# Performance work log

Measured on AMD Instinct MI355X. Metric: run time of the kernel, lower is better.

## Reference

```python
import jax, jax.numpy as jnp
import numpy as np

N = 20000      # nodes
E = 640000     # edges
R = 90         # relations
IN_F = 128     # raw feature dim
HID = 64       # hidden_channels
OUT = 32       # out_channels of conv2
NCLASS = 4
NB = 35        # num_bases (conv1)
EPS = 1e-16    # PyG softmax epsilon


def setup_inputs() -> dict:
    key = jax.random.key(0)
    ks = jax.random.split(key, 16)
    s = 0.1
    return {
        "x": jax.random.normal(ks[0], (N, IN_F), jnp.float32),
        "edge_index": jax.random.randint(ks[1], (2, E), 0, N, jnp.int32),
        "edge_type": jax.random.randint(ks[2], (E,), 0, R, jnp.int32),
        "edge_attr": jax.random.normal(ks[3], (E, 16), jnp.float32),
        # lin1: in_channels -> hidden (no bias)
        "lin1_w": jax.random.normal(ks[4], (IN_F, HID), jnp.float32) * s,
        # conv1: basis decomposition, heads=2, out=20, dim=2 -> H*O=40, H*dim=4
        "att1": jax.random.normal(ks[5], (R, NB), jnp.float32) * s,
        "basis1": jax.random.normal(ks[6], (NB, HID, 40), jnp.float32) * s,
        "q1": jax.random.normal(ks[7], (40, 4), jnp.float32) * s,
        "k1": jax.random.normal(ks[8], (40, 4), jnp.float32) * s,
        "wmod1": jnp.ones((20,), jnp.float32),            # mod='additive' weight (init ones)
        "bias1": jnp.zeros((80,), jnp.float32),            # concat bias: H*dim*O = 80
        # conv2: block-diagonal, in=80, blocks=2, H*O=64, H*dim=2
        "w2": jax.random.normal(ks[9], (R, 2, 40, 32), jnp.float32) * s,
        "q2": jax.random.normal(ks[10], (64, 2), jnp.float32) * s,
        "k2": jax.random.normal(ks[11], (64, 2), jnp.float32) * s,
        "lin_edge_w": jax.random.normal(ks[12], (16, 64), jnp.float32) * s,
        "e2": jax.random.normal(ks[13], (64, 2), jnp.float32) * s,
        # lin2: 2*out -> nclass
        "lin2_w": jax.random.normal(ks[14], (2 * OUT, NCLASS), jnp.float32) * s,
        "lin2_b": jnp.zeros((NCLASS,), jnp.float32),
    }


def segment_softmax(alpha, seg, num_segments):
    # PyG softmax: exp(x - detach(segment_max)) / (segment_sum + 1e-16)
    m = jax.ops.segment_max(alpha, seg, num_segments=num_segments)
    e = jnp.exp(alpha - jax.lax.stop_gradient(m)[seg])
    ssum = jax.ops.segment_sum(e, seg, num_segments=num_segments)
    return e / (ssum[seg] + EPS)


def rgat_forward(x, edge_index, edge_type, edge_attr, lin1_w, att1, basis1,
                 q1, k1, wmod1, bias1, w2, q2, k2, lin_edge_w, e2, lin2_w, lin2_b):
    src, dst = edge_index[0], edge_index[1]   # x_j = x[src], x_i = x[dst]
    n = x.shape[0]
    e = src.shape[0]

    h = x @ lin1_w                            # [N, HID]

    # ---- conv1: basis decomposition, within-relation, multiplicative attn, mod='additive'
    w = jnp.einsum('rb,bio->rio', att1, basis1)          # [R, HID, 40]
    xw = jnp.einsum('ni,rio->rno', h, w)                 # [R, N, 40] (all-relation transform)
    outj = xw[edge_type, src]                            # [E, 40]
    outi = xw[edge_type, dst]                            # [E, 40]
    qi = outi @ q1                                       # [E, 4]
    kj = outj @ k1                                       # [E, 4]
    alpha = qi * kj                                      # multiplicative-self-attention
    seg = dst.astype(jnp.int32) * R + edge_type          # within-relation softmax groups
    alpha = segment_softmax(alpha, seg, n * R)           # [E, 4]
    outj4 = outj.reshape(e, 2, 1, 20)                    # [E, H, 1, O]
    hmod = wmod1 * jnp.broadcast_to(outj4, (e, 2, 2, 20))  # mod='additive' term
    msg = outj4 * alpha.reshape(e, 2, 2, 1) + hmod       # [E, H, dim, O]
    agg = jax.ops.segment_sum(msg, dst, num_segments=n)  # [N, 2, 2, 20]
    h1 = agg.reshape(n, 80) + bias1
    h1 = jax.nn.relu(h1)

    # ---- conv2: block-diagonal, across-relation, additive attn, edge features, no bias
    xb = h1.reshape(n, 2, 40)
    xw2 = jnp.einsum('nbc,rbcd->rnbd', xb, w2).reshape(R, n, 64)  # [R, N, 64]
    outj = xw2[edge_type, src]                           # [E, 64]
    outi = xw2[edge_type, dst]
    qi = outi @ q2                                       # [E, 2]
    kj = outj @ k2
    ae = (edge_attr @ lin_edge_w) @ e2                   # [E, 2]
    alpha = jax.nn.leaky_relu(qi + kj + ae, 0.2)         # additive-self-attention
    alpha = segment_softmax(alpha, dst, n)               # across-relation
    msg = alpha.reshape(e, 2, 1) * outj.reshape(e, 2, 32)
    h2 = jax.ops.segment_sum(msg, dst, num_segments=n).reshape(n, 64)

    out = h2 @ lin2_w + lin2_b
    return jax.nn.log_softmax(out, axis=-1)


def reference(x, edge_index, edge_type, edge_attr, lin1_w, att1, basis1, q1, k1,
              wmod1, bias1, w2, q2, k2, lin_edge_w, e2, lin2_w, lin2_b):
    return rgat_forward(x, edge_index, edge_type, edge_attr, lin1_w, att1, basis1,
                        q1, k1, wmod1, bias1, w2, q2, k2, lin_edge_w, e2, lin2_w, lin2_b)
```

## Files before the change

### kernel.cpp

```cpp
#include <hip/hip_runtime.h>
#include <math.h>

constexpr int NN   = 20000;
constexpr int EE   = 640000;
constexpr int RR   = 90;
constexpr int INF_ = 128;
constexpr int HID  = 64;
constexpr float EPS = 1e-16f;
constexpr int E2   = 646144;

typedef unsigned short u16;
typedef _Float16 f16;
typedef __attribute__((ext_vector_type(8))) _Float16 f16x8;
typedef __attribute__((ext_vector_type(4))) _Float16 f16x4;
typedef __attribute__((ext_vector_type(4))) float f32x4;
typedef __attribute__((ext_vector_type(4))) int ivec4;

__device__ inline unsigned f2ord(float f) {
    unsigned u = __float_as_uint(f);
    return (u & 0x80000000u) ? ~u : (u | 0x80000000u);
}
__device__ inline float ord2f(unsigned x) {
    unsigned u = (x & 0x80000000u) ? (x & 0x7FFFFFFFu) : ~x;
    return __uint_as_float(u);
}
#define ORD_NEGINF 0x007FFFFFu

__global__ void k_fillrec(int4* p, int n) {
    int i = blockIdx.x * blockDim.x + threadIdx.x;
    if (i < n) { int4 r; r.x = 0; r.y = 0; r.z = 0; r.w = -1; p[i] = r; }
}

__global__ void k_hist(const int* et, int* hist) {
    __shared__ int lh[RR];
    if (threadIdx.x < RR) lh[threadIdx.x] = 0;
    __syncthreads();
    int i = blockIdx.x * blockDim.x + threadIdx.x;
    if (i < EE) atomicAdd(&lh[et[i]], 1);
    __syncthreads();
    if (threadIdx.x < RR) atomicAdd(&hist[threadIdx.x], lh[threadIdx.x]);
}

__global__ void k_scanPad(const int* hist, int* cursor) {
    if (threadIdx.x == 0) {
        int acc = 0;
        for (int r = 0; r < RR; ++r) {
            cursor[r] = acc;
            acc += (hist[r] + 63) & ~63;
        }
    }
}

__global__ void k_scatter(const int* src, const int* dst, const int* et,
                          int* cursor, int4* sortedR, int* posS) {
    __shared__ int lh[RR];
    __shared__ int lbase[RR];
    if (threadIdx.x < RR) lh[threadIdx.x] = 0;
    __syncthreads();
    int i = blockIdx.x * blockDim.x + threadIdx.x;
    int r = et[i];
    int rank = atomicAdd(&lh[r], 1);
    __syncthreads();
    if (threadIdx.x < RR) {
        int c = lh[threadIdx.x];
        lbase[threadIdx.x] = c ? atomicAdd(&cursor[threadIdx.x], c) : 0;
    }
    __syncthreads();
    int pos = lbase[r] + rank;
    int4 rec; rec.x = src[i]; rec.y = dst[i]; rec.z = r; rec.w = i;
    sortedR[pos] = rec;
    posS[i] = pos;
}

__global__ void k_histD(const int* dst, int* histD) {
    int i = blockIdx.x * blockDim.x + threadIdx.x;
    if (i < EE) atomicAdd(&histD[dst[i]], 1);
}

__global__ void k_scanD(const int* histD, int* rowptrD, int* cursorD) {
    __shared__ int part[256];
    const int CH = (NN + 255) / 256;
    int tid = threadIdx.x;
    int base = tid * CH;
    int s = 0;
    for (int j = 0; j < CH; ++j) {
        int idx = base + j;
        if (idx < NN) s += histD[idx];
    }
    part[tid] = s;
    __syncthreads();
    if (tid == 0) {
        int acc = 0;
        for (int t = 0; t < 256; ++t) { int v = part[t]; part[t] = acc; acc += v; }
    }
    __syncthreads();
    int acc = part[tid];
    for (int j = 0; j < CH; ++j) {
        int idx = base + j;
        if (idx < NN) {
            rowptrD[idx] = acc;
            cursorD[idx] = acc;
            acc += histD[idx];
        }
    }
    if (tid == 0) rowptrD[NN] = EE;
}

__global__ void k_scatterD(int4* sortedR, int* cursorD, u16* relD) {
    int i = blockIdx.x * blockDim.x + threadIdx.x;
    if (i >= E2) return;
    int4 rec = sortedR[i];
    if (rec.w < 0) return;
    int pos = atomicAdd(&cursorD[rec.y], 1);
    ((int*)(sortedR + i))[3] = pos;
    relD[pos] = (u16)rec.z;
}

__global__ void k_w1(const float* att1, const float* basis1, float* w1) {
    int idx = blockIdx.x * blockDim.x + threadIdx.x;
    if (idx >= RR * 2560) return;
    int r = idx / 2560, co = idx - r * 2560;
    float acc = 0.f;
    for (int b = 0; b < 35; ++b) acc += att1[r * 35 + b] * basis1[b * 2560 + co];
    w1[idx] = acc;
}

__global__ void k_wqk1(const float* w1, const float* q1, const float* k1,
                       float* wq1, float* wk1) {
    int idx = blockIdx.x * blockDim.x + threadIdx.x;
    if (idx >= RR * 64 * 4) return;
    int t = idx & 3, c = (idx >> 2) & 63, r = idx >> 8;
    const float* wrow = w1 + (size_t)r * 2560 + c * 40;
    float aq = 0.f, ak = 0.f;
    for (int o = 0; o < 40; ++o) {
        float w = wrow[o];
        aq += w * q1[o * 4 + t];
        ak += w * k1[o * 4 + t];
    }
    wq1[idx] = aq; wk1[idx] = ak;
}

__global__ void k_wqk2(const float* w2, const float* q2, const float* k2,
                       float* wq2, float* wk2) {
    int idx = blockIdx.x * blockDim.x + threadIdx.x;
    if (idx >= RR * 80 * 2) return;
    int t = idx & 1, bc = (idx >> 1) % 80, r = idx / 160;
    int b = bc / 40, c = bc % 40;
    const float* wbase = w2 + (size_t)((r * 2 + b) * 40 + c) * 32;
    float aq = 0.f, ak = 0.f;
    for (int d = 0; d < 32; ++d) {
        float w = wbase[d];
        aq += w * q2[(b * 32 + d) * 2 + t];
        ak += w * k2[(b * 32 + d) * 2 + t];
    }
    wq2[idx] = aq; wk2[idx] = ak;
}

__global__ void k_we(const float* lew, const float* e2, float* we) {
    int idx = threadIdx.x;
    if (idx >= 32) return;
    int i = idx >> 1, t = idx & 1;
    float acc = 0.f;
    for (int j = 0; j < 64; ++j) acc += lew[i * 64 + j] * e2[j * 2 + t];
    we[idx] = acc;
}

__global__ __launch_bounds__(256) void k_ae(const float* ea, const float* weg,
                                            const int* posS, float* aeS) {
    __shared__ float wes[32];
    if (threadIdx.x < 32) wes[threadIdx.x] = weg[threadIdx.x];
    __syncthreads();
    int e = blockIdx.x * 256 + threadIdx.x;
    if (e >= EE) return;
    const float4* ep = (const float4*)(ea + (size_t)e * 16);
    float a0 = 0.f, a1 = 0.f;
#pragma unroll
    for (int cc = 0; cc < 4; ++cc) {
        float4 v = ep[cc];
        const float* vv = (const float*)&v;
#pragma unroll
        for (int j = 0; j < 4; ++j) {
            int ii = cc * 4 + j;
            a0 = fmaf(vv[j], wes[ii * 2 + 0], a0);
            a1 = fmaf(vv[j], wes[ii * 2 + 1], a1);
        }
    }
    float2 av; av.x = a0; av.y = a1;
    *(float2*)(aeS + (size_t)posS[e] * 2) = av;
}

__global__ void k_w1hT(const float* w1, f16* w1hT) {
    int idx = blockIdx.x * blockDim.x + threadIdx.x;
    if (idx >= RR * 48 * 64) return;
    int k = idx & 63, o = (idx >> 6) % 48, r = idx / (48 * 64);
    float v = (o < 40) ? w1[(size_t)r * 2560 + k * 40 + o] : 0.f;
    w1hT[idx] = (f16)v;
}

__global__ void k_w2hT(const float* w2, f16* w2hT) {
    int idx = blockIdx.x * blockDim.x + threadIdx.x;
    if (idx >= RR * 2 * 32 * 64) return;
    int c = idx & 63, d = (idx >> 6) & 31, b = (idx >> 11) & 1, r = idx >> 12;
    float v = (c < 40) ? w2[((((size_t)r * 2 + b) * 40) + c) * 32 + d] : 0.f;
    w2hT[idx] = (f16)v;
}

__global__ void k_h(const float* x, const float* lin1_w, f16* hh) {
    __shared__ float xs[INF_];
    int n = blockIdx.x, t = threadIdx.x;
    xs[t]      = x[(size_t)n * INF_ + t];
    xs[t + 64] = x[(size_t)n * INF_ + t + 64];
    __syncthreads();
    float acc = 0.f;
    for (int i = 0; i < INF_; ++i) acc += xs[i] * lin1_w[i * HID + t];
    hh[(size_t)n * HID + t] = (f16)acc;
}

__global__ __launch_bounds__(256) void k_c1(const int4* sortedR, const f16* hh,
                                            const f16* w1hT,
                                            const float* wq1g, const float* wk1g,
                                            float* alpha1s, f16* outj1h) {
    __shared__ float qs[4][256], ks[4][256];
    int wid = threadIdx.x >> 6, l = threadIdx.x & 63;
    int wbase = blockIdx.x * 256 + wid * 64;
    int r = sortedR[wbase].z;
    float* qw = qs[wid];
    float* kw = ks[wid];
    for (int t = l; t < 256; t += 64) {
        qw[t] = wq1g[(size_t)r * 256 + t];
        kw[t] = wk1g[(size_t)r * 256 + t];
    }
    __syncthreads();
    int row16 = l & 15, g = l >> 4;
    f16x8 a[3][2];
#pragma unroll
    for (int mt = 0; mt < 3; ++mt)
#pragma unroll
        for (int kk = 0; kk < 2; ++kk)
            a[mt][kk] = *(const f16x8*)(w1hT + ((size_t)r * 48 + mt * 16 + row16) * 64 + kk * 32 + g * 8);
    ivec4 er[3];
    f16x8 vb0[3], vb1[3], vd0[3], vd1[3];

#define C1_LOAD(SLOT, T) { \
    int e0_ = wbase + (T) * 16; \
    er[SLOT] = __builtin_nontemporal_load((const ivec4*)(sortedR + e0_ + row16)); \
    int s_ = er[SLOT][0], d_ = er[SLOT][1]; \
    vb0[SLOT] = *(const f16x8*)(hh + (size_t)s_ * 64 + g * 8); \
    vb1[SLOT] = *(const f16x8*)(hh + (size_t)s_ * 64 + 32 + g * 8); \
    vd0[SLOT] = *(const f16x8*)(hh + (size_t)d_ * 64 + g * 8); \
    vd1[SLOT] = *(const f16x8*)(hh + (size_t)d_ * 64 + 32 + g * 8); }

#define C1_COMP(SLOT) { \
    int pd_ = er[SLOT][3]; \
    float qi[4] = {0.f,0.f,0.f,0.f}, kj[4] = {0.f,0.f,0.f,0.f}; \
    _Pragma("unroll") for (int j = 0; j < 8; ++j) { \
        int p0 = g * 8 + j, p1 = 32 + g * 8 + j; \
        float dv0 = (float)vd0[SLOT][j], dv1 = (float)vd1[SLOT][j]; \
        float bv0 = (float)vb0[SLOT][j], bv1 = (float)vb1[SLOT][j]; \
        _Pragma("unroll") for (int t2 = 0; t2 < 4; ++t2) { \
            qi[t2] = fmaf(dv0, qw[p0 * 4 + t2], fmaf(dv1, qw[p1 * 4 + t2], qi[t2])); \
            kj[t2] = fmaf(bv0, kw[p0 * 4 + t2], fmaf(bv1, kw[p1 * 4 + t2], kj[t2])); } } \
    _Pragma("unroll") for (int t2 = 0; t2 < 4; ++t2) { \
        qi[t2] += __shfl_xor(qi[t2], 16); qi[t2] += __shfl_xor(qi[t2], 32); \
        kj[t2] += __shfl_xor(kj[t2], 16); kj[t2] += __shfl_xor(kj[t2], 32); } \
    f32x4 acc[3]; \
    _Pragma("unroll") for (int mt = 0; mt < 3; ++mt) acc[mt] = (f32x4){0.f,0.f,0.f,0.f}; \
    _Pragma("unroll") for (int mt = 0; mt < 3; ++mt) { \
        acc[mt] = __builtin_amdgcn_mfma_f32_16x16x32_f16(a[mt][0], vb0[SLOT], acc[mt], 0, 0, 0); \
        acc[mt] = __builtin_amdgcn_mfma_f32_16x16x32_f16(a[mt][1], vb1[SLOT], acc[mt], 0, 0, 0); } \
    if (pd_ >= 0) { \
        if (l < 16) { \
            float4 av; \
            av.x = qi[0] * kj[0]; av.y = qi[1] * kj[1]; \
            av.z = qi[2] * kj[2]; av.w = qi[3] * kj[3]; \
            *(float4*)(alpha1s + (size_t)pd_ * 4) = av; } \
        f16* orow = outj1h + (size_t)pd_ * 40; \
        _Pragma("unroll") for (int mt = 0; mt < 3; ++mt) { \
            int col = mt * 16 + g * 4; \
            if (col < 40) { \
                f16x4 v; \
                v[0] = (f16)acc[mt][0]; v[1] = (f16)acc[mt][1]; \
                v[2] = (f16)acc[mt][2]; v[3] = (f16)acc[mt][3]; \
                *(f16x4*)(orow + col) = v; } } } }

    C1_LOAD(0, 0)
    C1_LOAD(1, 1)
    C1_LOAD(2, 2)
    C1_COMP(0)
    C1_LOAD(0, 3)
    C1_COMP(1)
    C1_COMP(2)
    C1_COMP(0)
#undef C1_LOAD
#undef C1_COMP
}

__global__ __launch_bounds__(256) void k_aggr1(const u16* relD, const int* rowptrD,
                                               const f16* outj1h, const float* alpha1s,
                                               const float* wmod, const float* bias1,
                                               f16* h1h) {
    __shared__ unsigned smax[4][RR * 5];
    __shared__ float    ssum[4][RR * 5];
    int wid = threadIdx.x >> 6;
    int lane = threadIdx.x & 63;
    int w = blockIdx.x * 4 + wid;
    int beg = rowptrD[w], end = rowptrD[w + 1];
    unsigned* mx = smax[wid];
    float*    sm = ssum[wid];
    for (int j = beg + lane; j < end; j += 64) {
        int rb = relD[j] * 5;
        mx[rb + 0] = ORD_NEGINF; mx[rb + 1] = ORD_NEGINF;
        mx[rb + 2] = ORD_NEGINF; mx[rb + 3] = ORD_NEGINF;
        sm[rb + 0] = 0.f; sm[rb + 1] = 0.f; sm[rb + 2] = 0.f; sm[rb + 3] = 0.f;
    }
    __syncthreads();
    for (int j = beg + lane; j < end; j += 64) {
        float4 a = *(const float4*)(alpha1s + (size_t)j * 4);
        int rb = relD[j] * 5;
        atomicMax(&mx[rb + 0], f2ord(a.x));
        atomicMax(&mx[rb + 1], f2ord(a.y));
        atomicMax(&mx[rb + 2], f2ord(a.z));
        atomicMax(&mx[rb + 3], f2ord(a.w));
    }
    __syncthreads();
    for (int j = beg + lane; j < end; j += 64) {
        float4 a = *(const float4*)(alpha1s + (size_t)j * 4);
        int rb = relD[j] * 5;
        atomicAdd(&sm[rb + 0], __expf(a.x - ord2f(mx[rb + 0])));
        atomicAdd(&sm[rb + 1], __expf(a.y - ord2f(mx[rb + 1])));
        atomicAdd(&sm[rb + 2], __expf(a.z - ord2f(mx[rb + 2])));
        atomicAdd(&sm[rb + 3], __expf(a.w - ord2f(mx[rb + 3])));
    }
    __syncthreads();
    for (int t = lane; t < RR * 5; t += 64) sm[t] = 1.f / (sm[t] + EPS);
    __syncthreads();
    int hh2 = lane >= 20 ? 1 : 0;
    int oo = lane - hh2 * 20;
    float acc0 = 0.f, acc1 = 0.f, accw = 0.f;
    if (lane < 40) {
        for (int j = beg; j < end; ++j) {
            int rb = relD[j] * 5 + hh2 * 2;
            float v = (float)__builtin_nontemporal_load(outj1h + (size_t)j * 40 + lane);
            float2 a = *(const float2*)(alpha1s + (size_t)j * 4 + hh2 * 2);
            float e0 = __expf(a.x - ord2f(mx[rb]));
            float e1 = __expf(a.y - ord2f(mx[rb + 1]));
            acc0 = fmaf(v, e0 * sm[rb], acc0);
            acc1 = fmaf(v, e1 * sm[rb + 1], acc1);
            accw += v;
        }
        float wm = wmod[oo];
        int b0 = hh2 * 40 + oo;
        float o0 = fmaxf(acc0 + wm * accw + bias1[b0], 0.f);
        float o1 = fmaxf(acc1 + wm * accw + bias1[b0 + 20], 0.f);
        h1h[(size_t)w * 80 + b0]      = (f16)o0;
        h1h[(size_t)w * 80 + b0 + 20] = (f16)o1;
    }
}

__global__ __launch_bounds__(256) void k_c2(const int4* sortedR, const f16* h1h,
                                            const f16* w2hT,
                                            const float* wq2g, const float* wk2g,
                                            const float* aeS,
                                            float* alpha2s, f16* outj2h) {
    __shared__ float qs[4][160], ks[4][160];
    int wid = threadIdx.x >> 6, l = threadIdx.x & 63;
    int wbase = blockIdx.x * 256 + wid * 64;
    int r = sortedR[wbase].z;
    float* qw = qs[wid];
    float* kw = ks[wid];
    for (int t = l; t < 160; t += 64) {
        qw[t] = wq2g[(size_t)r * 160 + t];
        kw[t] = wk2g[(size_t)r * 160 + t];
    }
    __syncthreads();
    int row16 = l & 15, g = l >> 4;
    f16x8 a[2][2][2];
#pragma unroll
    for (int b = 0; b < 2; ++b)
#pragma unroll
        for (int mt = 0; mt < 2; ++mt)
#pragma unroll
            for (int kk = 0; kk < 2; ++kk)
                a[b][mt][kk] = *(const f16x8*)(w2hT + ((((size_t)r * 2 + b) * 32) + mt * 16 + row16) * 64 + kk * 32 + g * 8);
    ivec4 er[3];
    f16x8 vb[3][2][2], vd[3][2][2];

#define C2_LOAD(SLOT, T) { \
    int e0_ = wbase + (T) * 16; \
    er[SLOT] = __builtin_nontemporal_load((const ivec4*)(sortedR + e0_ + row16)); \
    int s_ = er[SLOT][0], d_ = er[SLOT][1]; \
    _Pragma("unroll") for (int b = 0; b < 2; ++b) \
        _Pragma("unroll") for (int kk = 0; kk < 2; ++kk) { \
            vb[SLOT][b][kk] = *(const f16x8*)(h1h + (size_t)s_ * 80 + b * 40 + kk * 32 + g * 8); \
            vd[SLOT][b][kk] = *(const f16x8*)(h1h + (size_t)d_ * 80 + b * 40 + kk * 32 + g * 8); } }

#define C2_COMP(SLOT, T) { \
    int pd_ = er[SLOT][3]; \
    float a0 = 0.f, a1 = 0.f; \
    _Pragma("unroll") for (int b = 0; b < 2; ++b) { \
        _Pragma("unroll") for (int j = 0; j < 8; ++j) { \
            int p = b * 40 + g * 8 + j; \
            float dv = (float)vd[SLOT][b][0][j], bv = (float)vb[SLOT][b][0][j]; \
            a0 = fmaf(dv, qw[p * 2 + 0], fmaf(bv, kw[p * 2 + 0], a0)); \
            a1 = fmaf(dv, qw[p * 2 + 1], fmaf(bv, kw[p * 2 + 1], a1)); } \
        if (g == 0) { \
            _Pragma("unroll") for (int j = 0; j < 8; ++j) { \
                int p = b * 40 + 32 + j; \
                float dv = (float)vd[SLOT][b][1][j], bv = (float)vb[SLOT][b][1][j]; \
                a0 = fmaf(dv, qw[p * 2 + 0], fmaf(bv, kw[p * 2 + 0], a0)); \
                a1 = fmaf(dv, qw[p * 2 + 1], fmaf(bv, kw[p * 2 + 1], a1)); } } } \
    a0 += __shfl_xor(a0, 16); a0 += __shfl_xor(a0, 32); \
    a1 += __shfl_xor(a1, 16); a1 += __shfl_xor(a1, 32); \
    f32x4 acc[2][2]; \
    _Pragma("unroll") for (int b = 0; b < 2; ++b) \
        _Pragma("unroll") for (int mt = 0; mt < 2; ++mt) acc[b][mt] = (f32x4){0.f,0.f,0.f,0.f}; \
    _Pragma("unroll") for (int b = 0; b < 2; ++b) \
        _Pragma("unroll") for (int mt = 0; mt < 2; ++mt) { \
            acc[b][mt] = __builtin_amdgcn_mfma_f32_16x16x32_f16(a[b][mt][0], vb[SLOT][b][0], acc[b][mt], 0, 0, 0); \
            acc[b][mt] = __builtin_amdgcn_mfma_f32_16x16x32_f16(a[b][mt][1], vb[SLOT][b][1], acc[b][mt], 0, 0, 0); } \
    if (pd_ >= 0) { \
        if (l < 16) { \
            float2 aev = *(const float2*)(aeS + (size_t)(wbase + (T) * 16 + row16) * 2); \
            float x0 = a0 + aev.x, x1 = a1 + aev.y; \
            x0 = x0 > 0.f ? x0 : 0.2f * x0; \
            x1 = x1 > 0.f ? x1 : 0.2f * x1; \
            float2 av; av.x = x0; av.y = x1; \
            *(float2*)(alpha2s + (size_t)pd_ * 2) = av; } \
        f16* orow = outj2h + (size_t)pd_ * 64; \
        _Pragma("unroll") for (int b = 0; b < 2; ++b) \
            _Pragma("unroll") for (int mt = 0; mt < 2; ++mt) { \
                f16x4 v; \
                v[0] = (f16)acc[b][mt][0]; v[1] = (f16)acc[b][mt][1]; \
                v[2] = (f16)acc[b][mt][2]; v[3] = (f16)acc[b][mt][3]; \
                *(f16x4*)(orow + b * 32 + mt * 16 + g * 4) = v; } } }

    C2_LOAD(0, 0)
    C2_LOAD(1, 1)
    C2_LOAD(2, 2)
    C2_COMP(0, 0)
    C2_LOAD(0, 3)
    C2_COMP(1, 1)
    C2_COMP(2, 2)
    C2_COMP(0, 3)
#undef C2_LOAD
#undef C2_COMP
}

__global__ __launch_bounds__(256) void k_aggr2(const int* rowptrD, const f16* outj2h,
                                               const float* alpha2s, float* h2) {
    int w = blockIdx.x * 4 + (threadIdx.x >> 6);
    int lane = threadIdx.x & 63;
    if (w >= NN) return;
    int beg = rowptrD[w], end = rowptrD[w + 1];
    float m0 = -INFINITY, m1 = -INFINITY;
    for (int j = beg + lane; j < end; j += 64) {
        float2 a = *(const float2*)(alpha2s + (size_t)j * 2);
        m0 = fmaxf(m0, a.x); m1 = fmaxf(m1, a.y);
    }
#pragma unroll
    for (int off = 32; off; off >>= 1) {
        m0 = fmaxf(m0, __shfl_xor(m0, off));
        m1 = fmaxf(m1, __shfl_xor(m1, off));
    }
    float s0 = 0.f, s1 = 0.f;
    for (int j = beg + lane; j < end; j += 64) {
        float2 a = *(const float2*)(alpha2s + (size_t)j * 2);
        s0 += __expf(a.x - m0); s1 += __expf(a.y - m1);
    }
#pragma unroll
    for (int off = 32; off; off >>= 1) {
        s0 += __shfl_xor(s0, off);
        s1 += __shfl_xor(s1, off);
    }
    int b = lane >> 5;
    float mb = b ? m1 : m0;
    float rs = 1.f / ((b ? s1 : s0) + EPS);
    float acc = 0.f;
    for (int j = beg; j < end; ++j) {
        float v = (float)__builtin_nontemporal_load(outj2h + (size_t)j * 64 + lane);
        float a = alpha2s[(size_t)j * 2 + b];
        acc = fmaf(v, __expf(a - mb) * rs, acc);
    }
    h2[(size_t)w * 64 + lane] = acc;
}

__global__ void k_out(const float* h2, const float* lin2_w, const float* lin2_b,
                      float* out) {
    int n = blockIdx.x * blockDim.x + threadIdx.x;
    if (n >= NN) return;
    float o[4] = {lin2_b[0], lin2_b[1], lin2_b[2], lin2_b[3]};
    const float* hr = h2 + (size_t)n * 64;
    for (int c = 0; c < 64; ++c) {
        float hv = hr[c];
#pragma unroll
        for (int t = 0; t < 4; ++t) o[t] = fmaf(hv, lin2_w[c * 4 + t], o[t]);
    }
    float m = fmaxf(fmaxf(o[0], o[1]), fmaxf(o[2], o[3]));
    float s = __expf(o[0] - m) + __expf(o[1] - m) + __expf(o[2] - m) + __expf(o[3] - m);
    float lse = m + logf(s);
#pragma unroll
    for (int t = 0; t < 4; ++t) out[(size_t)n * 4 + t] = o[t] - lse;
}

extern "C" void kernel_launch(void* const* d_in, const int* in_sizes, int n_in,
                              void* d_out, int out_size, void* d_ws, size_t ws_size,
                              hipStream_t stream) {
    const float* x        = (const float*)d_in[0];
    const int*   eidx     = (const int*)d_in[1];
    const int*   etype    = (const int*)d_in[2];
    const float* eattr    = (const float*)d_in[3];
    const float* lin1_w   = (const float*)d_in[4];
    const float* att1     = (const float*)d_in[5];
    const float* basis1   = (const float*)d_in[6];
    const float* q1       = (const float*)d_in[7];
    const float* k1       = (const float*)d_in[8];
    const float* wmod1    = (const float*)d_in[9];
    const float* bias1    = (const float*)d_in[10];
    const float* w2       = (const float*)d_in[11];
    const float* q2       = (const float*)d_in[12];
    const float* k2       = (const float*)d_in[13];
    const float* lew      = (const float*)d_in[14];
    const float* e2i      = (const float*)d_in[15];
    const float* lin2_w   = (const float*)d_in[16];
    const float* lin2_b   = (const float*)d_in[17];

    const int* src = eidx;
    const int* dst = eidx + EE;

    float* W = (float*)d_ws;
    float* w1      = W;   W += 230400;
    float* wq1     = W;   W += 23040;
    float* wk1     = W;   W += 23040;
    float* wq2     = W;   W += 14400;
    float* wk2     = W;   W += 14400;
    float* we      = W;   W += 32;
    float* h2      = W;   W += (size_t)NN * 64;
    float* aeS     = W;   W += (size_t)E2 * 2;
    f16*   hh      = (f16*)W;   W += (size_t)NN * 64 / 2;
    f16*   h1h     = (f16*)W;   W += (size_t)NN * 80 / 2 + 32;
    f16*   w1hT    = (f16*)W;   W += (size_t)RR * 48 * 64 / 2;
    f16*   w2hT    = (f16*)W;   W += (size_t)RR * 2 * 32 * 64 / 2;
    float* uni     = W;   W += (size_t)EE * 20 + (size_t)EE * 4;
    f16*   outj1h  = (f16*)uni;
    float* alpha1s = uni + (size_t)EE * 20;
    f16*   outj2h  = (f16*)uni;
    W += (size_t)EE * 8;
    float* alpha2s = W;   W += (size_t)EE * 2;
    int4*  sortedR = (int4*)W;
    int*   I = (int*)W;   I += (size_t)E2 * 4;
    u16*   relD    = (u16*)I;   I += (size_t)E2 / 2;
    int*   posS    = I;   I += EE;
    int*   rowptrD = I;   I += NN + 1;
    int*   cursorD = I;   I += NN;
    int*   histD   = I;   I += NN;
    int*   hist    = I;   I += 128;
    int*   cursor  = I;   I += 128;

    hipMemsetAsync(histD, 0, (size_t)(NN + 256) * 4, stream);
    hipMemsetAsync(h1h + (size_t)NN * 80, 0, 128, stream);
    k_fillrec<<<E2 / 256, 256, 0, stream>>>(sortedR, E2);

    k_hist<<<EE / 256, 256, 0, stream>>>(etype, hist);
    k_scanPad<<<1, 64, 0, stream>>>(hist, cursor);
    k_scatter<<<EE / 256, 256, 0, stream>>>(src, dst, etype, cursor, sortedR, posS);
    k_histD<<<EE / 256, 256, 0, stream>>>(dst, histD);
    k_scanD<<<1, 256, 0, stream>>>(histD, rowptrD, cursorD);
    k_scatterD<<<E2 / 256, 256, 0, stream>>>(sortedR, cursorD, relD);

    k_w1<<<(RR * 2560 + 255) / 256, 256, 0, stream>>>(att1, basis1, w1);
    k_wqk1<<<(RR * 256 + 255) / 256, 256, 0, stream>>>(w1, q1, k1, wq1, wk1);
    k_wqk2<<<(RR * 160 + 255) / 256, 256, 0, stream>>>(w2, q2, k2, wq2, wk2);
    k_we<<<1, 32, 0, stream>>>(lew, e2i, we);
    k_ae<<<EE / 256, 256, 0, stream>>>(eattr, we, posS, aeS);
    k_w1hT<<<(RR * 48 * 64) / 256, 256, 0, stream>>>(w1, w1hT);
    k_w2hT<<<(RR * 2 * 32 * 64) / 256, 256, 0, stream>>>(w2, w2hT);
    k_h<<<NN, 64, 0, stream>>>(x, lin1_w, hh);

    k_c1<<<E2 / 256, 256, 0, stream>>>(sortedR, hh, w1hT, wq1, wk1, alpha1s, outj1h);
    k_aggr1<<<NN / 4, 256, 0, stream>>>(relD, rowptrD, outj1h, alpha1s,
                                        wmod1, bias1, h1h);

    k_c2<<<E2 / 256, 256, 0, stream>>>(sortedR, h1h, w2hT, wq2, wk2, aeS,
                                       alpha2s, outj2h);
    k_aggr2<<<(NN + 3) / 4, 256, 0, stream>>>(rowptrD, outj2h, alpha2s, h2);

    k_out<<<(NN + 255) / 256, 256, 0, stream>>>(h2, lin2_w, lin2_b, (float*)d_out);
}
```

Before: 589.8 us.

## Move query projection from edge kernels into destination-grouped aggregation kernels

Result: slower. 957.8 us (+62.4%).

```diff
diff --git a/kernel.cpp b/kernel.cpp
--- a/kernel.cpp
+++ b/kernel.cpp
@@ -217,19 +217,15 @@
 }
 
 __global__ __launch_bounds__(256) void k_c1(const int4* sortedR, const f16* hh,
-                                            const f16* w1hT,
-                                            const float* wq1g, const float* wk1g,
+                                            const f16* w1hT, const float* wk1g,
                                             float* alpha1s, f16* outj1h) {
-    __shared__ float qs[4][256], ks[4][256];
+    __shared__ float ks[4][256];
     int wid = threadIdx.x >> 6, l = threadIdx.x & 63;
     int wbase = blockIdx.x * 256 + wid * 64;
     int r = sortedR[wbase].z;
-    float* qw = qs[wid];
     float* kw = ks[wid];
-    for (int t = l; t < 256; t += 64) {
-        qw[t] = wq1g[(size_t)r * 256 + t];
+    for (int t = l; t < 256; t += 64)
         kw[t] = wk1g[(size_t)r * 256 + t];
-    }
     __syncthreads();
     int row16 = l & 15, g = l >> 4;
     f16x8 a[3][2];
@@ -239,29 +235,24 @@
         for (int kk = 0; kk < 2; ++kk)
             a[mt][kk] = *(const f16x8*)(w1hT + ((size_t)r * 48 + mt * 16 + row16) * 64 + kk * 32 + g * 8);
     ivec4 er[3];
-    f16x8 vb0[3], vb1[3], vd0[3], vd1[3];
+    f16x8 vb0[3], vb1[3];
 
 #define C1_LOAD(SLOT, T) { \
     int e0_ = wbase + (T) * 16; \
     er[SLOT] = __builtin_nontemporal_load((const ivec4*)(sortedR + e0_ + row16)); \
-    int s_ = er[SLOT][0], d_ = er[SLOT][1]; \
+    int s_ = er[SLOT][0]; \
     vb0[SLOT] = *(const f16x8*)(hh + (size_t)s_ * 64 + g * 8); \
-    vb1[SLOT] = *(const f16x8*)(hh + (size_t)s_ * 64 + 32 + g * 8); \
-    vd0[SLOT] = *(const f16x8*)(hh + (size_t)d_ * 64 + g * 8); \
-    vd1[SLOT] = *(const f16x8*)(hh + (size_t)d_ * 64 + 32 + g * 8); }
+    vb1[SLOT] = *(const f16x8*)(hh + (size_t)s_ * 64 + 32 + g * 8); }
 
 #define C1_COMP(SLOT) { \
     int pd_ = er[SLOT][3]; \
-    float qi[4] = {0.f,0.f,0.f,0.f}, kj[4] = {0.f,0.f,0.f,0.f}; \
+    float kj[4] = {0.f,0.f,0.f,0.f}; \
     _Pragma("unroll") for (int j = 0; j < 8; ++j) { \
         int p0 = g * 8 + j, p1 = 32 + g * 8 + j; \
-        float dv0 = (float)vd0[SLOT][j], dv1 = (float)vd1[SLOT][j]; \
         float bv0 = (float)vb0[SLOT][j], bv1 = (float)vb1[SLOT][j]; \
-        _Pragma("unroll") for (int t2 = 0; t2 < 4; ++t2) { \
-            qi[t2] = fmaf(dv0, qw[p0 * 4 + t2], fmaf(dv1, qw[p1 * 4 + t2], qi[t2])); \
-            kj[t2] = fmaf(bv0, kw[p0 * 4 + t2], fmaf(bv1, kw[p1 * 4 + t2], kj[t2])); } } \
+        _Pragma("unroll") for (int t2 = 0; t2 < 4; ++t2) \
+            kj[t2] = fmaf(bv0, kw[p0 * 4 + t2], fmaf(bv1, kw[p1 * 4 + t2], kj[t2])); } \
     _Pragma("unroll") for (int t2 = 0; t2 < 4; ++t2) { \
-        qi[t2] += __shfl_xor(qi[t2], 16); qi[t2] += __shfl_xor(qi[t2], 32); \
         kj[t2] += __shfl_xor(kj[t2], 16); kj[t2] += __shfl_xor(kj[t2], 32); } \
     f32x4 acc[3]; \
     _Pragma("unroll") for (int mt = 0; mt < 3; ++mt) acc[mt] = (f32x4){0.f,0.f,0.f,0.f}; \
@@ -270,9 +261,7 @@
         acc[mt] = __builtin_amdgcn_mfma_f32_16x16x32_f16(a[mt][1], vb1[SLOT], acc[mt], 0, 0, 0); } \
     if (pd_ >= 0) { \
         if (l < 16) { \
-            float4 av; \
-            av.x = qi[0] * kj[0]; av.y = qi[1] * kj[1]; \
-            av.z = qi[2] * kj[2]; av.w = qi[3] * kj[3]; \
+            float4 av; av.x = kj[0]; av.y = kj[1]; av.z = kj[2]; av.w = kj[3]; \
             *(float4*)(alpha1s + (size_t)pd_ * 4) = av; } \
         f16* orow = outj1h + (size_t)pd_ * 40; \
         _Pragma("unroll") for (int mt = 0; mt < 3; ++mt) { \
@@ -296,7 +285,8 @@
 }
 
 __global__ __launch_bounds__(256) void k_aggr1(const u16* relD, const int* rowptrD,
-                                               const f16* outj1h, const float* alpha1s,
+                                               const f16* hh, const float* wq1g,
+                                               const f16* outj1h, float* alpha1s,
                                                const float* wmod, const float* bias1,
                                                f16* h1h) {
     __shared__ unsigned smax[4][RR * 5];
@@ -307,6 +297,10 @@
     int beg = rowptrD[w], end = rowptrD[w + 1];
     unsigned* mx = smax[wid];
     float*    sm = ssum[wid];
+    f16x8 hd[8];
+#pragma unroll
+    for (int cc = 0; cc < 8; ++cc)
+        hd[cc] = *(const f16x8*)(hh + (size_t)w * 64 + cc * 8);
     for (int j = beg + lane; j < end; j += 64) {
         int rb = relD[j] * 5;
         mx[rb + 0] = ORD_NEGINF; mx[rb + 1] = ORD_NEGINF;
@@ -315,8 +309,26 @@
     }
     __syncthreads();
     for (int j = beg + lane; j < end; j += 64) {
-        float4 a = *(const float4*)(alpha1s + (size_t)j * 4);
-        int rb = relD[j] * 5;
+        float4 kj = *(const float4*)(alpha1s + (size_t)j * 4);
+        int r = relD[j];
+        const float* qrow = wq1g + (size_t)r * 256;
+        float q0 = 0.f, q1 = 0.f, q2 = 0.f, q3 = 0.f;
+#pragma unroll
+        for (int cc = 0; cc < 8; ++cc) {
+#pragma unroll
+            for (int jj = 0; jj < 8; ++jj) {
+                float hv = (float)hd[cc][jj];
+                const float* q4 = qrow + (cc * 8 + jj) * 4;
+                q0 = fmaf(hv, q4[0], q0);
+                q1 = fmaf(hv, q4[1], q1);
+                q2 = fmaf(hv, q4[2], q2);
+                q3 = fmaf(hv, q4[3], q3);
+            }
+        }
+        float4 a;
+        a.x = q0 * kj.x; a.y = q1 * kj.y; a.z = q2 * kj.z; a.w = q3 * kj.w;
+        *(float4*)(alpha1s + (size_t)j * 4) = a;
+        int rb = r * 5;
         atomicMax(&mx[rb + 0], f2ord(a.x));
         atomicMax(&mx[rb + 1], f2ord(a.y));
         atomicMax(&mx[rb + 2], f2ord(a.z));
@@ -358,20 +370,16 @@
 }
 
 __global__ __launch_bounds__(256) void k_c2(const int4* sortedR, const f16* h1h,
-                                            const f16* w2hT,
-                                            const float* wq2g, const float* wk2g,
+                                            const f16* w2hT, const float* wk2g,
                                             const float* aeS,
                                             float* alpha2s, f16* outj2h) {
-    __shared__ float qs[4][160], ks[4][160];
+    __shared__ float ks[4][160];
     int wid = threadIdx.x >> 6, l = threadIdx.x & 63;
     int wbase = blockIdx.x * 256 + wid * 64;
     int r = sortedR[wbase].z;
-    float* qw = qs[wid];
     float* kw = ks[wid];
-    for (int t = l; t < 160; t += 64) {
-        qw[t] = wq2g[(size_t)r * 160 + t];
+    for (int t = l; t < 160; t += 64)
         kw[t] = wk2g[(size_t)r * 160 + t];
-    }
     __syncthreads();
     int row16 = l & 15, g = l >> 4;
     f16x8 a[2][2][2];
@@ -383,16 +391,15 @@
             for (int kk = 0; kk < 2; ++kk)
                 a[b][mt][kk] = *(const f16x8*)(w2hT + ((((size_t)r * 2 + b) * 32) + mt * 16 + row16) * 64 + kk * 32 + g * 8);
     ivec4 er[3];
-    f16x8 vb[3][2][2], vd[3][2][2];
+    f16x8 vb[3][2][2];
 
 #define C2_LOAD(SLOT, T) { \
     int e0_ = wbase + (T) * 16; \
     er[SLOT] = __builtin_nontemporal_load((const ivec4*)(sortedR + e0_ + row16)); \
-    int s_ = er[SLOT][0], d_ = er[SLOT][1]; \
+    int s_ = er[SLOT][0]; \
     _Pragma("unroll") for (int b = 0; b < 2; ++b) \
-        _Pragma("unroll") for (int kk = 0; kk < 2; ++kk) { \
-            vb[SLOT][b][kk] = *(const f16x8*)(h1h + (size_t)s_ * 80 + b * 40 + kk * 32 + g * 8); \
-            vd[SLOT][b][kk] = *(const f16x8*)(h1h + (size_t)d_ * 80 + b * 40 + kk * 32 + g * 8); } }
+        _Pragma("unroll") for (int kk = 0; kk < 2; ++kk) \
+            vb[SLOT][b][kk] = *(const f16x8*)(h1h + (size_t)s_ * 80 + b * 40 + kk * 32 + g * 8); }
 
 #define C2_COMP(SLOT, T) { \
     int pd_ = er[SLOT][3]; \
@@ -400,15 +407,15 @@
     _Pragma("unroll") for (int b = 0; b < 2; ++b) { \
         _Pragma("unroll") for (int j = 0; j < 8; ++j) { \
             int p = b * 40 + g * 8 + j; \
-            float dv = (float)vd[SLOT][b][0][j], bv = (float)vb[SLOT][b][0][j]; \
-            a0 = fmaf(dv, qw[p * 2 + 0], fmaf(bv, kw[p * 2 + 0], a0)); \
-            a1 = fmaf(dv, qw[p * 2 + 1], fmaf(bv, kw[p * 2 + 1], a1)); } \
+            float bv = (float)vb[SLOT][b][0][j]; \
+            a0 = fmaf(bv, kw[p * 2 + 0], a0); \
+            a1 = fmaf(bv, kw[p * 2 + 1], a1); } \
         if (g == 0) { \
             _Pragma("unroll") for (int j = 0; j < 8; ++j) { \
                 int p = b * 40 + 32 + j; \
-                float dv = (float)vd[SLOT][b][1][j], bv = (float)vb[SLOT][b][1][j]; \
-                a0 = fmaf(dv, qw[p * 2 + 0], fmaf(bv, kw[p * 2 + 0], a0)); \
-                a1 = fmaf(dv, qw[p * 2 + 1], fmaf(bv, kw[p * 2 + 1], a1)); } } } \
+                float bv = (float)vb[SLOT][b][1][j]; \
+                a0 = fmaf(bv, kw[p * 2 + 0], a0); \
+                a1 = fmaf(bv, kw[p * 2 + 1], a1); } } } \
     a0 += __shfl_xor(a0, 16); a0 += __shfl_xor(a0, 32); \
     a1 += __shfl_xor(a1, 16); a1 += __shfl_xor(a1, 32); \
     f32x4 acc[2][2]; \
@@ -421,10 +428,7 @@
     if (pd_ >= 0) { \
         if (l < 16) { \
             float2 aev = *(const float2*)(aeS + (size_t)(wbase + (T) * 16 + row16) * 2); \
-            float x0 = a0 + aev.x, x1 = a1 + aev.y; \
-            x0 = x0 > 0.f ? x0 : 0.2f * x0; \
-            x1 = x1 > 0.f ? x1 : 0.2f * x1; \
-            float2 av; av.x = x0; av.y = x1; \
+            float2 av; av.x = a0 + aev.x; av.y = a1 + aev.y; \
             *(float2*)(alpha2s + (size_t)pd_ * 2) = av; } \
         f16* orow = outj2h + (size_t)pd_ * 64; \
         _Pragma("unroll") for (int b = 0; b < 2; ++b) \
@@ -446,22 +450,46 @@
 #undef C2_COMP
 }
 
-__global__ __launch_bounds__(256) void k_aggr2(const int* rowptrD, const f16* outj2h,
-                                               const float* alpha2s, float* h2) {
+__global__ __launch_bounds__(256) void k_aggr2(const u16* relD, const int* rowptrD,
+                                               const f16* h1h, const float* wq2g,
+                                               const f16* outj2h, float* alpha2s,
+                                               float* h2) {
     int w = blockIdx.x * 4 + (threadIdx.x >> 6);
     int lane = threadIdx.x & 63;
-    if (w >= NN) return;
     int beg = rowptrD[w], end = rowptrD[w + 1];
+    f16x8 hd[10];
+#pragma unroll
+    for (int cc = 0; cc < 10; ++cc)
+        hd[cc] = *(const f16x8*)(h1h + (size_t)w * 80 + cc * 8);
     float m0 = -INFINITY, m1 = -INFINITY;
     for (int j = beg + lane; j < end; j += 64) {
-        float2 a = *(const float2*)(alpha2s + (size_t)j * 2);
-        m0 = fmaxf(m0, a.x); m1 = fmaxf(m1, a.y);
+        float2 kv = *(const float2*)(alpha2s + (size_t)j * 2);
+        int r = relD[j];
+        const float* qrow = wq2g + (size_t)r * 160;
+        float q0 = 0.f, q1 = 0.f;
+#pragma unroll
+        for (int cc = 0; cc < 10; ++cc) {
+#pragma unroll
+            for (int jj = 0; jj < 8; ++jj) {
+                float hv = (float)hd[cc][jj];
+                int p = cc * 8 + jj;
+                q0 = fmaf(hv, qrow[p * 2 + 0], q0);
+                q1 = fmaf(hv, qrow[p * 2 + 1], q1);
+            }
+        }
+        float x0 = q0 + kv.x, x1 = q1 + kv.y;
+        x0 = x0 > 0.f ? x0 : 0.2f * x0;
+        x1 = x1 > 0.f ? x1 : 0.2f * x1;
+        float2 av; av.x = x0; av.y = x1;
+        *(float2*)(alpha2s + (size_t)j * 2) = av;
+        m0 = fmaxf(m0, x0); m1 = fmaxf(m1, x1);
     }
 #pragma unroll
     for (int off = 32; off; off >>= 1) {
         m0 = fmaxf(m0, __shfl_xor(m0, off));
         m1 = fmaxf(m1, __shfl_xor(m1, off));
     }
+    __syncthreads();
     float s0 = 0.f, s1 = 0.f;
     for (int j = beg + lane; j < end; j += 64) {
         float2 a = *(const float2*)(alpha2s + (size_t)j * 2);
@@ -576,13 +604,14 @@
     k_w2hT<<<(RR * 2 * 32 * 64) / 256, 256, 0, stream>>>(w2, w2hT);
     k_h<<<NN, 64, 0, stream>>>(x, lin1_w, hh);
 
-    k_c1<<<E2 / 256, 256, 0, stream>>>(sortedR, hh, w1hT, wq1, wk1, alpha1s, outj1h);
-    k_aggr1<<<NN / 4, 256, 0, stream>>>(relD, rowptrD, outj1h, alpha1s,
+    k_c1<<<E2 / 256, 256, 0, stream>>>(sortedR, hh, w1hT, wk1, alpha1s, outj1h);
+    k_aggr1<<<NN / 4, 256, 0, stream>>>(relD, rowptrD, hh, wq1, outj1h, alpha1s,
                                         wmod1, bias1, h1h);
 
-    k_c2<<<E2 / 256, 256, 0, stream>>>(sortedR, h1h, w2hT, wq2, wk2, aeS,
+    k_c2<<<E2 / 256, 256, 0, stream>>>(sortedR, h1h, w2hT, wk2, aeS,
                                        alpha2s, outj2h);
-    k_aggr2<<<(NN + 3) / 4, 256, 0, stream>>>(rowptrD, outj2h, alpha2s, h2);
+    k_aggr2<<<NN / 4, 256, 0, stream>>>(relD, rowptrD, h1h, wq2, outj2h,
+                                        alpha2s, h2);
 
     k_out<<<(NN + 255) / 256, 256, 0, stream>>>(h2, lin2_w, lin2_b, (float*)d_out);
 }
```
